# Performance work log

Hardware: AMD Instinct MI355X
Metric: run time of the kernel (lower is better)

The kernel has to match this reference:

```python
import jax, jax.numpy as jnp
import numpy as np

B, P, CIN = 512, 64, 512       # batch, h*w feature positions, resnet18 channels
HID, EMB, NCLS, T = 512, 512, 96, 30


def setup_inputs() -> dict:
    key = jax.random.key(0)
    ks = jax.random.split(key, 16)
    s = 0.02
    return {
        "features": jax.random.normal(ks[0], (B, P, CIN), jnp.float32),
        "targets": jax.random.randint(ks[1], (B, T), 0, NCLS),
        "max_length": T,
        "Wfc": jax.random.normal(ks[2], (HID, CIN), jnp.float32) * s,
        "bfc": jnp.zeros((HID,), jnp.float32),
        "emb_table": jax.random.normal(ks[3], (NCLS, EMB), jnp.float32) * s,
        "Wa": jax.random.normal(ks[4], (HID, HID + EMB), jnp.float32) * s,
        "ba": jnp.zeros((HID,), jnp.float32),
        "Wc": jax.random.normal(ks[5], (HID, HID + EMB), jnp.float32) * s,
        "bc": jnp.zeros((HID,), jnp.float32),
        "Wih": jax.random.normal(ks[6], (4 * HID, HID), jnp.float32) * s,
        "Whh": jax.random.normal(ks[7], (4 * HID, HID), jnp.float32) * s,
        "bih": jnp.zeros((4 * HID,), jnp.float32),
        "bhh": jnp.zeros((4 * HID,), jnp.float32),
        "Wo": jax.random.normal(ks[8], (NCLS, HID), jnp.float32) * s,
        "bo": jnp.zeros((NCLS,), jnp.float32),
    }


def reference(features, targets, max_length, Wfc, bfc, emb_table, Wa, ba,
              Wc, bc, Wih, Whh, bih, bhh, Wo, bo):
    b = features.shape[0]
    hid = Wfc.shape[0]
    feats = features @ Wfc.T + bfc                       # [b, P, hid]
    # teacher forcing: input at t=0 is token 0, then targets[:, t-1]
    in_ids = jnp.concatenate(
        [jnp.zeros((b, 1), targets.dtype), targets[:, : max_length - 1]], axis=1)
    emb_seq = emb_table[in_ids].transpose(1, 0, 2)       # [T, b, emb]

    def step(carry, emb):
        h, c = carry
        # first softmax is over the hidden dim (as in the original module)
        a = jax.nn.softmax(jnp.concatenate([h, emb], -1) @ Wa.T + ba, axis=-1)  # [b,hid]
        scores = jnp.einsum('bph,bh->bp', feats, a)      # [b, P]
        w = jax.nn.softmax(scores, axis=-1)
        ctx = jnp.einsum('bp,bph->bh', w, feats)         # [b, hid]
        x = jnp.concatenate([emb, ctx], -1) @ Wc.T + bc  # [b, hid]
        gates = x @ Wih.T + bih + h @ Whh.T + bhh        # [b, 4*hid]
        i, f, g, o = jnp.split(gates, 4, axis=-1)        # torch gate order i,f,g,o
        c_new = jax.nn.sigmoid(f) * c + jax.nn.sigmoid(i) * jnp.tanh(g)
        h_new = jax.nn.sigmoid(o) * jnp.tanh(c_new)
        out = h_new @ Wo.T + bo                          # [b, ncls]
        return (h_new, c_new), out

    h0 = jnp.zeros((b, hid), feats.dtype)
    (_, _), outs = jax.lax.scan(step, (h0, h0), emb_seq)
    return outs.transpose(1, 0, 2)                       # [b, T, ncls]
```

## Files before the change

kernel.cpp:

```cpp
#include <hip/hip_runtime.h>
#include <math.h>

static constexpr int BATCH = 512;
static constexpr int PPOS  = 64;
static constexpr int HIDC  = 512;

typedef __attribute__((ext_vector_type(8))) short bf8;
typedef __attribute__((ext_vector_type(4))) short s4v;
typedef __attribute__((ext_vector_type(4))) float f4;

static __device__ __forceinline__ float sigmoidf_(float x) { return 1.f / (1.f + expf(-x)); }

static __device__ __forceinline__ short f2bf(float x) {
  unsigned u = __float_as_uint(x);
  u = u + 0x7FFF + ((u >> 16) & 1);
  return (short)(u >> 16);
}
static __device__ __forceinline__ float bf2f(short s) {
  return __uint_as_float(((unsigned)(unsigned short)s) << 16);
}

__global__ void transpose_k(const float* __restrict__ src, float* __restrict__ dst, int R, int C, int ld) {
  __shared__ float tile[32][33];
  int c0 = blockIdx.x * 32, r0 = blockIdx.y * 32;
  int x = threadIdx.x;
  for (int yy = threadIdx.y; yy < 32; yy += 8) {
    int r = r0 + yy, c = c0 + x;
    if (r < R && c < C) tile[yy][x] = src[(size_t)r * ld + c];
  }
  __syncthreads();
  for (int yy = threadIdx.y; yy < 32; yy += 8) {
    int c = c0 + yy, r = r0 + x;
    if (r < R && c < C) dst[(size_t)c * R + r] = tile[x][yy];
  }
}

__global__ void bfuse_k(const float* __restrict__ Wih, const float* __restrict__ bc,
                        const float* __restrict__ bih, const float* __restrict__ bhh,
                        float* __restrict__ bf) {
  int n = blockIdx.x * 256 + threadIdx.x;
  float s = bih[n] + bhh[n];
  const float* w = Wih + (size_t)n * 512;
  for (int m = 0; m < 512; m++) s += w[m] * bc[m];
  bf[n] = s;
}

__global__ void split_k(const float* __restrict__ src, short* __restrict__ hi, short* __restrict__ lo, int n) {
  int i = blockIdx.x * 256 + threadIdx.x;
  if (i < n) {
    float x = src[i];
    short h = f2bf(x);
    hi[i] = h;
    lo[i] = f2bf(x - bf2f(h));
  }
}

__global__ void fsplit_k(const float* __restrict__ src, short* __restrict__ hi, short* __restrict__ lo) {
  int i = blockIdx.x * 256 + threadIdx.x;
  float4 v = ((const float4*)src)[i];
  float a[4] = {v.x, v.y, v.z, v.w};
  s4v h4, l4;
#pragma unroll
  for (int j = 0; j < 4; j++) {
    short h = f2bf(a[j]);
    h4[j] = h;
    l4[j] = f2bf(a[j] - bf2f(h));
  }
  ((s4v*)hi)[i] = h4;
  ((s4v*)lo)[i] = l4;
}

__global__ void pack_split_k(const float* __restrict__ src, int ld,
                             short* __restrict__ hi, short* __restrict__ lo) {
  int idx = blockIdx.x * 256 + threadIdx.x;
  int j = idx & 7, lane = (idx >> 3) & 63, kf = (idx >> 9) & 15, cg = idx >> 13;
  int n = cg * 16 + (lane & 15);
  int k = kf * 32 + ((lane >> 4) << 3) + j;
  float v = src[(size_t)n * ld + k];
  short h = f2bf(v);
  hi[idx] = h;
  lo[idx] = f2bf(v - bf2f(h));
}

__global__ void build_btg_pack_k(const float* __restrict__ tmp, const float* __restrict__ Whh,
                                 short* __restrict__ hi, short* __restrict__ lo) {
  int idx = blockIdx.x * 256 + threadIdx.x;
  int j = idx & 7, lane = (idx >> 3) & 63, kf = (idx >> 9) & 31, cg = idx >> 14;
  int cp = cg * 16 + (lane & 15);
  int k = kf * 32 + ((lane >> 4) << 3) + j;
  int jj = cp >> 2, g = cp & 3;
  int n = g * 512 + jj;
  float v = (k < 512) ? tmp[(size_t)(512 + k) * 2048 + n] : Whh[(size_t)n * 512 + (k - 512)];
  short h = f2bf(v);
  hi[idx] = h;
  lo[idx] = f2bf(v - bf2f(h));
}

__global__ __launch_bounds__(256) void gemb_k(const float* __restrict__ emb_table, const float* __restrict__ tmp,
                                              const float* __restrict__ bfused, float* __restrict__ Gemb_p) {
  __shared__ float emb_s[4][512];
  int tid = threadIdx.x;
  int n0 = blockIdx.x * 256;
  int e0 = blockIdx.y * 4;
  for (int i = tid; i < 2048; i += 256)
    emb_s[i >> 9][i & 511] = emb_table[(size_t)(e0 + (i >> 9)) * 512 + (i & 511)];
  __syncthreads();
  int n = n0 + tid;
  float acc[4] = {};
  for (int k = 0; k < 512; k++) {
    float w = tmp[(size_t)k * 2048 + n];
#pragma unroll
    for (int e = 0; e < 4; e++) acc[e] += emb_s[e][k] * w;
  }
  int cp = (n & 511) * 4 + (n >> 9);
  float b = bfused[n];
#pragma unroll
  for (int e = 0; e < 4; e++) Gemb_p[(size_t)(e0 + e) * 2048 + cp] = acc[e] + b;
}

__global__ __launch_bounds__(256) void za_k(const float* __restrict__ emb_table, const float* __restrict__ WaT_emb,
                                            const float* __restrict__ ba, float* __restrict__ Za) {
  __shared__ float emb_s[4][512];
  int tid = threadIdx.x;
  int n0 = blockIdx.x * 256;
  int e0 = blockIdx.y * 4;
  for (int i = tid; i < 2048; i += 256)
    emb_s[i >> 9][i & 511] = emb_table[(size_t)(e0 + (i >> 9)) * 512 + (i & 511)];
  __syncthreads();
  int n = n0 + tid;
  float acc[4] = {};
  for (int k = 0; k < 512; k++) {
    float w = WaT_emb[(size_t)k * 512 + n];
#pragma unroll
    for (int e = 0; e < 4; e++) acc[e] += emb_s[e][k] * w;
  }
  float b = ba[n];
#pragma unroll
  for (int e = 0; e < 4; e++) Za[(size_t)(e0 + e) * 512 + n] = acc[e] + b;
}

__global__ __launch_bounds__(256) void feats_mfma_k(const short* __restrict__ Fh, const short* __restrict__ Fl,
                                                    const short* __restrict__ Ph, const short* __restrict__ Pl,
                                                    const float* __restrict__ bias, float* __restrict__ C) {
  int blk = blockIdx.x;
  int xt = (blk >> 3) & 3;
  int ytile = (blk >> 5) * 8 + (blk & 7);
  int row0 = ytile * 64, col0 = xt * 128;
  int tid = threadIdx.x;
  int lane = tid & 63, wave = tid >> 6;
  int wm = (wave & 1) * 32, wn = (wave >> 1) * 64;
  int r15 = lane & 15, q8 = (lane >> 4) * 8;
  const short* a0h = Fh + (size_t)(row0 + wm + r15) * 512 + q8;
  const short* a0l = Fl + (size_t)(row0 + wm + r15) * 512 + q8;
  int cg0 = (col0 + wn) >> 4;
  const short* pbh = Ph + (size_t)cg0 * 8192 + lane * 8;
  const short* pbl = Pl + (size_t)cg0 * 8192 + lane * 8;
  bf8 cah[2], cal[2], cbh[4], cbl[4], nah[2], nal[2], nbh[4], nbl[4];
  cah[0] = *(const bf8*)a0h; cah[1] = *(const bf8*)(a0h + 16 * 512);
  cal[0] = *(const bf8*)a0l; cal[1] = *(const bf8*)(a0l + 16 * 512);
#pragma unroll
  for (int c = 0; c < 4; c++) {
    cbh[c] = *(const bf8*)(pbh + c * 8192);
    cbl[c] = *(const bf8*)(pbl + c * 8192);
  }
  f4 acc[2][4] = {};
#pragma unroll 4
  for (int kt = 0; kt < 16; kt++) {
    if (kt + 1 < 16) {
      int o = (kt + 1) * 32;
      nah[0] = *(const bf8*)(a0h + o); nah[1] = *(const bf8*)(a0h + 16 * 512 + o);
      nal[0] = *(const bf8*)(a0l + o); nal[1] = *(const bf8*)(a0l + 16 * 512 + o);
#pragma unroll
      for (int c = 0; c < 4; c++) {
        nbh[c] = *(const bf8*)(pbh + c * 8192 + (kt + 1) * 512);
        nbl[c] = *(const bf8*)(pbl + c * 8192 + (kt + 1) * 512);
      }
    }
#pragma unroll
    for (int r = 0; r < 2; r++)
#pragma unroll
      for (int c = 0; c < 4; c++) {
        acc[r][c] = __builtin_amdgcn_mfma_f32_16x16x32_bf16(cah[r], cbh[c], acc[r][c], 0, 0, 0);
        acc[r][c] = __builtin_amdgcn_mfma_f32_16x16x32_bf16(cal[r], cbh[c], acc[r][c], 0, 0, 0);
        acc[r][c] = __builtin_amdgcn_mfma_f32_16x16x32_bf16(cah[r], cbl[c], acc[r][c], 0, 0, 0);
      }
#pragma unroll
    for (int r = 0; r < 2; r++) { cah[r] = nah[r]; cal[r] = nal[r]; }
#pragma unroll
    for (int c = 0; c < 4; c++) { cbh[c] = nbh[c]; cbl[c] = nbl[c]; }
  }
#pragma unroll
  for (int r = 0; r < 2; r++)
#pragma unroll
    for (int c = 0; c < 4; c++) {
      int col = col0 + wn + c * 16 + r15;
      float bv = bias[col];
#pragma unroll
      for (int i = 0; i < 4; i++) {
        int row = row0 + wm + r * 16 + (lane >> 4) * 4 + i;
        C[(size_t)row * 512 + col] = acc[r][c][i] + bv;
      }
    }
}

__global__ __launch_bounds__(256) void tmp_mfma_k(const float* __restrict__ A,
                                                  const short* __restrict__ BTh, const short* __restrict__ BTl,
                                                  float* __restrict__ C) {
  __shared__ short Ah[2][64][40], Al[2][64][40], Bh[2][128][40], Bl[2][128][40];
  int row0 = blockIdx.y * 64, col0 = blockIdx.x * 128;
  int tid = threadIdx.x;
  int lane = tid & 63, wave = tid >> 6;
  int wm = (wave & 1) * 32, wn = (wave >> 1) * 64;
  int r15 = lane & 15, q8 = (lane >> 4) * 8;
  int smA = tid >> 2, skA = (tid & 3) * 8;
  int smB = tid >> 1, skB = (tid & 1) * 16;
  const float* Ap = A + (size_t)(row0 + smA) * 512 + skA;
  const short* Bhp = BTh + (size_t)(col0 + smB) * 512 + skB;
  const short* Blp = BTl + (size_t)(col0 + smB) * 512 + skB;
  float4 a0 = *(const float4*)Ap, a1 = *(const float4*)(Ap + 4);
  bf8 bh0 = *(const bf8*)Bhp, bh1 = *(const bf8*)(Bhp + 8);
  bf8 bl0 = *(const bf8*)Blp, bl1 = *(const bf8*)(Blp + 8);
  f4 acc[2][4] = {};
  for (int kt = 0; kt < 16; kt++) {
    int buf = kt & 1;
    {
      float av[8] = {a0.x, a0.y, a0.z, a0.w, a1.x, a1.y, a1.z, a1.w};
      bf8 ahv, alv;
#pragma unroll
      for (int i = 0; i < 8; i++) {
        short h = f2bf(av[i]);
        ahv[i] = h;
        alv[i] = f2bf(av[i] - bf2f(h));
      }
      *(bf8*)&Ah[buf][smA][skA] = ahv;
      *(bf8*)&Al[buf][smA][skA] = alv;
      *(bf8*)&Bh[buf][smB][skB] = bh0;
      *(bf8*)&Bh[buf][smB][skB + 8] = bh1;
      *(bf8*)&Bl[buf][smB][skB] = bl0;
      *(bf8*)&Bl[buf][smB][skB + 8] = bl1;
    }
    if (kt + 1 < 16) {
      Ap += 32; Bhp += 32; Blp += 32;
      a0 = *(const float4*)Ap; a1 = *(const float4*)(Ap + 4);
      bh0 = *(const bf8*)Bhp; bh1 = *(const bf8*)(Bhp + 8);
      bl0 = *(const bf8*)Blp; bl1 = *(const bf8*)(Blp + 8);
    }
    __syncthreads();
    bf8 fah[2], fal[2], fbh[4], fbl[4];
#pragma unroll
    for (int r = 0; r < 2; r++) {
      fah[r] = *(const bf8*)&Ah[buf][wm + r * 16 + r15][q8];
      fal[r] = *(const bf8*)&Al[buf][wm + r * 16 + r15][q8];
    }
#pragma unroll
    for (int c = 0; c < 4; c++) {
      fbh[c] = *(const bf8*)&Bh[buf][wn + c * 16 + r15][q8];
      fbl[c] = *(const bf8*)&Bl[buf][wn + c * 16 + r15][q8];
    }
#pragma unroll
    for (int r = 0; r < 2; r++)
#pragma unroll
      for (int c = 0; c < 4; c++) {
        acc[r][c] = __builtin_amdgcn_mfma_f32_16x16x32_bf16(fah[r], fbh[c], acc[r][c], 0, 0, 0);
        acc[r][c] = __builtin_amdgcn_mfma_f32_16x16x32_bf16(fal[r], fbh[c], acc[r][c], 0, 0, 0);
        acc[r][c] = __builtin_amdgcn_mfma_f32_16x16x32_bf16(fah[r], fbl[c], acc[r][c], 0, 0, 0);
      }
  }
#pragma unroll
  for (int r = 0; r < 2; r++)
#pragma unroll
    for (int c = 0; c < 4; c++) {
      int col = col0 + wn + c * 16 + r15;
#pragma unroll
      for (int i = 0; i < 4; i++) {
        int row = row0 + wm + r * 16 + (lane >> 4) * 4 + i;
        C[(size_t)row * 2048 + col] = acc[r][c][i];
      }
    }
}

__global__ __launch_bounds__(256) void z_mfma_k(const short* __restrict__ h_hi, const short* __restrict__ h_lo,
                                                const short* __restrict__ Ph, const short* __restrict__ Pl,
                                                float* __restrict__ zbuf) {
  int tid = threadIdx.x;
  int lane = tid & 63, wave = tid >> 6;
  int wm = (wave & 1) * 16, wn = (wave >> 1) * 16;
  int r15 = lane & 15, q4 = (lane >> 4) * 4, q8 = (lane >> 4) * 8;
  int row0 = blockIdx.y * 32, col0 = blockIdx.x * 32;
  int kz = blockIdx.z * 256;
  const short* ah = h_hi + (size_t)(row0 + wm + r15) * 512 + kz + q8;
  const short* al = h_lo + (size_t)(row0 + wm + r15) * 512 + kz + q8;
  int cg = (col0 + wn) >> 4;
  const short* pbh = Ph + (size_t)cg * 8192 + (size_t)blockIdx.z * 4096 + lane * 8;
  const short* pbl = Pl + (size_t)cg * 8192 + (size_t)blockIdx.z * 4096 + lane * 8;
  bf8 cah = *(const bf8*)ah, cal = *(const bf8*)al;
  bf8 cbh = *(const bf8*)pbh, cbl = *(const bf8*)pbl;
  bf8 nah, nal, nbh, nbl;
  f4 acc = {};
#pragma unroll
  for (int kt = 0; kt < 8; kt++) {
    if (kt + 1 < 8) {
      nah = *(const bf8*)(ah + (kt + 1) * 32);
      nal = *(const bf8*)(al + (kt + 1) * 32);
      nbh = *(const bf8*)(pbh + (kt + 1) * 512);
      nbl = *(const bf8*)(pbl + (kt + 1) * 512);
    }
    acc = __builtin_amdgcn_mfma_f32_16x16x32_bf16(cah, cbh, acc, 0, 0, 0);
    acc = __builtin_amdgcn_mfma_f32_16x16x32_bf16(cal, cbh, acc, 0, 0, 0);
    acc = __builtin_amdgcn_mfma_f32_16x16x32_bf16(cah, cbl, acc, 0, 0, 0);
    cah = nah; cal = nal; cbh = nbh; cbl = nbl;
  }
  float* zo = zbuf + (size_t)blockIdx.z * (512 * 512);
  int col = col0 + wn + r15;
#pragma unroll
  for (int i = 0; i < 4; i++)
    zo[(size_t)(row0 + wm + q4 + i) * 512 + col] = acc[i];
}

__global__ __launch_bounds__(512) void attn_fin_k(const float* __restrict__ zbuf,
                                                  const int* __restrict__ targets, int t, int T,
                                                  const float* __restrict__ Za, const float* __restrict__ feats,
                                                  short* __restrict__ ctx_hi, short* __restrict__ ctx_lo) {
  __shared__ float a_s[512];
  __shared__ float redm[8], reds[8];
  __shared__ float sc_s[64];
  __shared__ float w_s[64];
  __shared__ float cpart[8][512];
  int tid = threadIdx.x;
  int wid = tid >> 6, lane = tid & 63;
  int b = blockIdx.x;
  int id = (t == 0) ? 0 : targets[b * T + t - 1];

  const float4* fbase = (const float4*)(feats + (size_t)b * PPOS * 512);
  float4 f1[8], f2[8];
#pragma unroll
  for (int q = 0; q < 8; q++) {
    int p = wid * 8 + q;
    f1[q] = fbase[(size_t)p * 128 + lane];
    f2[q] = fbase[(size_t)p * 128 + 64 + lane];
  }

  float zv = zbuf[(size_t)b * 512 + tid] + zbuf[(size_t)(512 * 512) + b * 512 + tid]
           + Za[(size_t)id * 512 + tid];
  float m = zv;
#pragma unroll
  for (int off = 32; off; off >>= 1) m = fmaxf(m, __shfl_xor(m, off, 64));
  if (lane == 0) redm[wid] = m;
  __syncthreads();
  float M = redm[0];
#pragma unroll
  for (int w = 1; w < 8; w++) M = fmaxf(M, redm[w]);
  float e = expf(zv - M);
  float s = e;
#pragma unroll
  for (int off = 32; off; off >>= 1) s += __shfl_xor(s, off, 64);
  if (lane == 0) reds[wid] = s;
  __syncthreads();
  float S = 0.f;
#pragma unroll
  for (int w = 0; w < 8; w++) S += reds[w];
  a_s[tid] = e * (1.f / S);
  __syncthreads();

  float4 a1 = ((const float4*)a_s)[lane];
  float4 a2 = ((const float4*)a_s)[lane + 64];
#pragma unroll
  for (int q = 0; q < 8; q++) {
    float d = f1[q].x * a1.x + f1[q].y * a1.y + f1[q].z * a1.z + f1[q].w * a1.w
            + f2[q].x * a2.x + f2[q].y * a2.y + f2[q].z * a2.z + f2[q].w * a2.w;
#pragma unroll
    for (int off = 32; off; off >>= 1) d += __shfl_xor(d, off, 64);
    if (lane == 0) sc_s[wid * 8 + q] = d;
  }
  __syncthreads();

  if (wid == 0) {
    float v = sc_s[lane];
    float mm = v;
#pragma unroll
    for (int off = 32; off; off >>= 1) mm = fmaxf(mm, __shfl_xor(mm, off, 64));
    float ee = expf(v - mm);
    float ss = ee;
#pragma unroll
    for (int off = 32; off; off >>= 1) ss += __shfl_xor(ss, off, 64);
    w_s[lane] = ee / ss;
  }
  __syncthreads();

  float4 c1 = {0.f, 0.f, 0.f, 0.f}, c2 = {0.f, 0.f, 0.f, 0.f};
#pragma unroll
  for (int q = 0; q < 8; q++) {
    float wp = w_s[wid * 8 + q];
    c1.x += wp * f1[q].x; c1.y += wp * f1[q].y; c1.z += wp * f1[q].z; c1.w += wp * f1[q].w;
    c2.x += wp * f2[q].x; c2.y += wp * f2[q].y; c2.z += wp * f2[q].z; c2.w += wp * f2[q].w;
  }
  ((float4*)&cpart[wid][0])[lane] = c1;
  ((float4*)&cpart[wid][256])[lane] = c2;
  __syncthreads();

  float acc = 0.f;
#pragma unroll
  for (int w = 0; w < 8; w++) acc += cpart[w][tid];
  short hh = f2bf(acc);
  ctx_hi[(size_t)b * 512 + tid] = hh;
  ctx_lo[(size_t)b * 512 + tid] = f2bf(acc - bf2f(hh));
}

__global__ __launch_bounds__(256) void gates_mfma_k(const short* __restrict__ ctx_hi, const short* __restrict__ ctx_lo,
                                                    const short* __restrict__ h_hi_in, const short* __restrict__ h_lo_in,
                                                    const int* __restrict__ targets, int t, int T,
                                                    const short* __restrict__ Ph, const short* __restrict__ Pl,
                                                    const float* __restrict__ Gemb_p,
                                                    float* __restrict__ cbuf, float* __restrict__ h_new,
                                                    short* __restrict__ h_hi_out, short* __restrict__ h_lo_out) {
  __shared__ short Ah[2][32][72], Al[2][32][72];
  __shared__ float Cs[32][68];
  int tid = threadIdx.x;
  int lane = tid & 63, wave = tid >> 6;
  int wn = wave * 16;
  int r15 = lane & 15, q8 = (lane >> 4) * 8;
  int row0 = blockIdx.y * 32, col0 = blockIdx.x * 64;
  int smA = tid >> 3, skA = (tid & 7) * 8;
  const short* actx_h = ctx_hi + (size_t)(row0 + smA) * 512;
  const short* actx_l = ctx_lo + (size_t)(row0 + smA) * 512;
  const short* ahst_h = h_hi_in + (size_t)(row0 + smA) * 512;
  const short* ahst_l = h_lo_in + (size_t)(row0 + smA) * 512;
  int cg = (col0 >> 4) + wave;
  const short* pbh = Ph + (size_t)cg * 16384 + lane * 8;
  const short* pbl = Pl + (size_t)cg * 16384 + lane * 8;
  bf8 ah = *(const bf8*)(actx_h + skA), al = *(const bf8*)(actx_l + skA);
  bf8 bhc[2], blc[2], bhn[2], bln[2];
#pragma unroll
  for (int ks = 0; ks < 2; ks++) {
    bhc[ks] = *(const bf8*)(pbh + ks * 512);
    blc[ks] = *(const bf8*)(pbl + ks * 512);
  }
  f4 acc[2] = {};
#pragma unroll 2
  for (int kt = 0; kt < 16; kt++) {
    int buf = kt & 1;
    *(bf8*)&Ah[buf][smA][skA] = ah;
    *(bf8*)&Al[buf][smA][skA] = al;
    if (kt + 1 < 16) {
      int kk = (kt + 1) * 64 + skA;
      if (kk < 512) {
        ah = *(const bf8*)(actx_h + kk);
        al = *(const bf8*)(actx_l + kk);
      } else {
        ah = *(const bf8*)(ahst_h + kk - 512);
        al = *(const bf8*)(ahst_l + kk - 512);
      }
#pragma unroll
      for (int ks = 0; ks < 2; ks++) {
        bhn[ks] = *(const bf8*)(pbh + ((kt + 1) * 2 + ks) * 512);
        bln[ks] = *(const bf8*)(pbl + ((kt + 1) * 2 + ks) * 512);
      }
    }
    __syncthreads();
#pragma unroll
    for (int ks = 0; ks < 2; ks++) {
      bf8 fah[2], fal[2];
#pragma unroll
      for (int r = 0; r < 2; r++) {
        fah[r] = *(const bf8*)&Ah[buf][r * 16 + r15][ks * 32 + q8];
        fal[r] = *(const bf8*)&Al[buf][r * 16 + r15][ks * 32 + q8];
      }
#pragma unroll
      for (int r = 0; r < 2; r++) {
        acc[r] = __builtin_amdgcn_mfma_f32_16x16x32_bf16(fah[r], bhc[ks], acc[r], 0, 0, 0);
        acc[r] = __builtin_amdgcn_mfma_f32_16x16x32_bf16(fal[r], bhc[ks], acc[r], 0, 0, 0);
        acc[r] = __builtin_amdgcn_mfma_f32_16x16x32_bf16(fah[r], blc[ks], acc[r], 0, 0, 0);
      }
    }
#pragma unroll
    for (int ks = 0; ks < 2; ks++) { bhc[ks] = bhn[ks]; blc[ks] = bln[ks]; }
  }
#pragma unroll
  for (int r = 0; r < 2; r++)
#pragma unroll
    for (int i = 0; i < 4; i++)
      Cs[r * 16 + (lane >> 4) * 4 + i][wn + r15] = acc[r][i];
  __syncthreads();
#pragma unroll
  for (int it = 0; it < 2; it++) {
    int idx = it * 256 + tid;
    int row = idx >> 4, jj = idx & 15;
    int b = row0 + row;
    int jg = (col0 >> 2) + jj;
    int id = (t == 0) ? 0 : targets[b * T + t - 1];
    float4 g4 = *(const float4*)(Gemb_p + (size_t)id * 2048 + col0 + jj * 4);
    float ig = sigmoidf_(Cs[row][jj * 4 + 0] + g4.x);
    float fg = sigmoidf_(Cs[row][jj * 4 + 1] + g4.y);
    float gg = tanhf(Cs[row][jj * 4 + 2] + g4.z);
    float og = sigmoidf_(Cs[row][jj * 4 + 3] + g4.w);
    float cn = fg * cbuf[(size_t)b * 512 + jg] + ig * gg;
    float hn = og * tanhf(cn);
    cbuf[(size_t)b * 512 + jg] = cn;
    h_new[(size_t)b * 512 + jg] = hn;
    short hh = f2bf(hn);
    h_hi_out[(size_t)b * 512 + jg] = hh;
    h_lo_out[(size_t)b * 512 + jg] = f2bf(hn - bf2f(hh));
  }
}

__global__ __launch_bounds__(256) void out_gemm_k(const float* __restrict__ h_hist, const float* __restrict__ WoT,
                                                  const float* __restrict__ bo, float* __restrict__ out, int T) {
  __shared__ float As[16][68];
  __shared__ float Bs[16][96];
  int tid = threadIdx.x;
  int tx = tid & 15, ty = tid >> 4;
  int row0 = blockIdx.x * 64;
  float acc[4][6] = {};
  for (int k0 = 0; k0 < 512; k0 += 16) {
    {
      int r = tid >> 2;
      int kk = (tid & 3) * 4;
      float4 v = *(const float4*)(h_hist + (size_t)(row0 + r) * 512 + k0 + kk);
      As[kk + 0][r] = v.x; As[kk + 1][r] = v.y; As[kk + 2][r] = v.z; As[kk + 3][r] = v.w;
    }
#pragma unroll
    for (int i = 0; i < 6; i++) {
      int e = tid + 256 * i;
      int kb = e / 96, n = e - kb * 96;
      Bs[kb][n] = WoT[(size_t)(k0 + kb) * 96 + n];
    }
    __syncthreads();
#pragma unroll
    for (int q = 0; q < 16; q++) {
      float av[4], bvv[6];
#pragma unroll
      for (int i = 0; i < 4; i++) av[i] = As[q][ty * 4 + i];
#pragma unroll
      for (int j = 0; j < 6; j++) bvv[j] = Bs[q][tx * 6 + j];
#pragma unroll
      for (int i = 0; i < 4; i++)
#pragma unroll
        for (int j = 0; j < 6; j++) acc[i][j] += av[i] * bvv[j];
    }
    __syncthreads();
  }
#pragma unroll
  for (int i = 0; i < 4; i++)
#pragma unroll
    for (int j = 0; j < 6; j++) {
      int row = row0 + ty * 4 + i;
      int tt = row >> 9, bb = row & 511;
      int cc = tx * 6 + j;
      out[((size_t)bb * T + tt) * 96 + cc] = acc[i][j] + bo[cc];
    }
}

extern "C" void kernel_launch(void* const* d_in, const int* in_sizes, int n_in,
                              void* d_out, int out_size, void* d_ws, size_t ws_size,
                              hipStream_t stream) {
  const float* features  = (const float*)d_in[0];
  const int*   targets   = (const int*)d_in[1];
  const float* Wfc       = (const float*)d_in[3];
  const float* bfc       = (const float*)d_in[4];
  const float* emb_table = (const float*)d_in[5];
  const float* Wa        = (const float*)d_in[6];
  const float* ba        = (const float*)d_in[7];
  const float* Wc        = (const float*)d_in[8];
  const float* bc        = (const float*)d_in[9];
  const float* Wih       = (const float*)d_in[10];
  const float* Whh       = (const float*)d_in[11];
  const float* bih       = (const float*)d_in[12];
  const float* bhh       = (const float*)d_in[13];
  const float* Wo        = (const float*)d_in[14];
  const float* bo        = (const float*)d_in[15];
  float* out = (float*)d_out;
  int T = in_sizes[1] / BATCH;

  char* base = (char*)d_ws;
  auto alloc = [&](size_t bytes) -> char* {
    char* p = base;
    base += (bytes + 255) & ~(size_t)255;
    return p;
  };
  float* feats   = (float*)alloc((size_t)BATCH * PPOS * HIDC * 4);
  short* f_hi    = (short*)alloc((size_t)BATCH * PPOS * HIDC * 2);
  short* f_lo    = (short*)alloc((size_t)BATCH * PPOS * HIDC * 2);
  float* WaT_emb = (float*)alloc(512 * 512 * 4);
  float* WcT     = (float*)alloc(1024 * 512 * 4);
  float* tmp     = (float*)alloc((size_t)1024 * 2048 * 4);
  short* Wih_hi  = (short*)alloc((size_t)2048 * 512 * 2);
  short* Wih_lo  = (short*)alloc((size_t)2048 * 512 * 2);
  short* PBTg_hi = (short*)alloc((size_t)2048 * 1024 * 2);
  short* PBTg_lo = (short*)alloc((size_t)2048 * 1024 * 2);
  short* Pfc_hi  = (short*)alloc(512 * 512 * 2);
  short* Pfc_lo  = (short*)alloc(512 * 512 * 2);
  short* Pwa_hi  = (short*)alloc(512 * 512 * 2);
  short* Pwa_lo  = (short*)alloc(512 * 512 * 2);
  float* Gemb_p  = (float*)alloc(96 * 2048 * 4);
  float* Za      = (float*)alloc(96 * 512 * 4);
  float* bfused  = (float*)alloc(2048 * 4);
  float* WoT     = (float*)alloc(512 * 96 * 4);
  float* cbuf    = (float*)alloc(BATCH * HIDC * 4);
  float* zbuf    = (float*)alloc((size_t)2 * BATCH * HIDC * 4);
  short* ctx_hi  = (short*)alloc(BATCH * HIDC * 2);
  short* ctx_lo  = (short*)alloc(BATCH * HIDC * 2);
  short* h_hi    = (short*)alloc(BATCH * HIDC * 2);
  short* h_lo    = (short*)alloc(BATCH * HIDC * 2);
  float* h_hist  = (float*)alloc((size_t)T * BATCH * HIDC * 4);

  dim3 tb(32, 8);
  transpose_k<<<dim3(16, 16), tb, 0, stream>>>(Wa + 512, WaT_emb, 512, 512, 1024);
  transpose_k<<<dim3(32, 16), tb, 0, stream>>>(Wc, WcT, 512, 1024, 1024);
  transpose_k<<<dim3(16, 3),  tb, 0, stream>>>(Wo, WoT, 96, 512, 512);

  split_k<<<(2048 * 512) / 256, 256, 0, stream>>>(Wih, Wih_hi, Wih_lo, 2048 * 512);
  pack_split_k<<<(512 * 512) / 256, 256, 0, stream>>>(Wfc, 512, Pfc_hi, Pfc_lo);
  pack_split_k<<<(512 * 512) / 256, 256, 0, stream>>>(Wa, 1024, Pwa_hi, Pwa_lo);
  fsplit_k<<<(BATCH * PPOS * HIDC / 4) / 256, 256, 0, stream>>>(features, f_hi, f_lo);

  tmp_mfma_k<<<dim3(16, 16), 256, 0, stream>>>(WcT, Wih_hi, Wih_lo, tmp);

  bfuse_k<<<8, 256, 0, stream>>>(Wih, bc, bih, bhh, bfused);
  build_btg_pack_k<<<(2048 * 1024) / 256, 256, 0, stream>>>(tmp, Whh, PBTg_hi, PBTg_lo);
  gemb_k<<<dim3(8, 24), 256, 0, stream>>>(emb_table, tmp, bfused, Gemb_p);
  za_k<<<dim3(2, 24), 256, 0, stream>>>(emb_table, WaT_emb, ba, Za);

  feats_mfma_k<<<2048, 256, 0, stream>>>(f_hi, f_lo, Pfc_hi, Pfc_lo, bfc, feats);

  hipMemsetAsync(cbuf, 0, (size_t)BATCH * HIDC * 4, stream);
  hipMemsetAsync(h_hi, 0, (size_t)BATCH * HIDC * 2, stream);
  hipMemsetAsync(h_lo, 0, (size_t)BATCH * HIDC * 2, stream);

  for (int t = 0; t < T; t++) {
    float* h_new = h_hist + (size_t)t * BATCH * HIDC;
    z_mfma_k<<<dim3(16, 16, 2), 256, 0, stream>>>(h_hi, h_lo, Pwa_hi, Pwa_lo, zbuf);
    attn_fin_k<<<512, 512, 0, stream>>>(zbuf, targets, t, T, Za, feats, ctx_hi, ctx_lo);
    gates_mfma_k<<<dim3(32, 16), 256, 0, stream>>>(ctx_hi, ctx_lo, h_hi, h_lo, targets, t, T,
                                                   PBTg_hi, PBTg_lo, Gemb_p, cbuf, h_new, h_hi, h_lo);
  }
  out_gemm_k<<<(T * BATCH) / 64, 256, 0, stream>>>(h_hist, WoT, bo, out, T);
}
```

Baseline: 1.448 ms.

## Stage MFMA A-operands via direct global-to-LDS loads with XOR swizzle

Three MFMA kernels (feats, z, gates) now load the A operand (hi/lo bf16 split) straight from global memory into double-buffered shared memory with global_load_lds. Each kernel then reads its fragments from an XOR-swizzled layout, which replaces per-lane register loads or register-staged LDS stores. The aim is to cut VGPR pressure and load-issue overhead and to avoid LDS bank conflicts, since padding is dropped in favour of the swizzle. In exchange, feats and z gain a __syncthreads per k-iteration, and correctness depends on the async LDS load being complete at the barrier.

New measurement: 1.469 ms. About the same (+1.4%).

```diff
diff --git a/kernel.cpp b/kernel.cpp
--- a/kernel.cpp
+++ b/kernel.cpp
@@ -18,6 +18,11 @@
 }
 static __device__ __forceinline__ float bf2f(short s) {
   return __uint_as_float(((unsigned)(unsigned short)s) << 16);
+}
+
+static __device__ __forceinline__ void gld16(const short* g, short* l) {
+  __builtin_amdgcn_global_load_lds((const __attribute__((address_space(1))) unsigned int*)g,
+                                   (__attribute__((address_space(3))) unsigned int*)l, 16, 0, 0);
 }
 
 __global__ void transpose_k(const float* __restrict__ src, float* __restrict__ dst, int R, int C, int ld) {
@@ -142,6 +147,7 @@
 __global__ __launch_bounds__(256) void feats_mfma_k(const short* __restrict__ Fh, const short* __restrict__ Fl,
                                                     const short* __restrict__ Ph, const short* __restrict__ Pl,
                                                     const float* __restrict__ bias, float* __restrict__ C) {
+  __shared__ short Ah[2][64][32], Al[2][64][32];
   int blk = blockIdx.x;
   int xt = (blk >> 3) & 3;
   int ytile = (blk >> 5) * 8 + (blk & 7);
@@ -149,43 +155,52 @@
   int tid = threadIdx.x;
   int lane = tid & 63, wave = tid >> 6;
   int wm = (wave & 1) * 32, wn = (wave >> 1) * 64;
-  int r15 = lane & 15, q8 = (lane >> 4) * 8;
-  const short* a0h = Fh + (size_t)(row0 + wm + r15) * 512 + q8;
-  const short* a0l = Fl + (size_t)(row0 + wm + r15) * 512 + q8;
+  int r15 = lane & 15;
+  int srow = 16 * wave + (lane >> 2);
+  int sg = (lane & 3) ^ (srow & 3);
+  const short* gAh = Fh + (size_t)(row0 + srow) * 512 + (sg << 3);
+  const short* gAl = Fl + (size_t)(row0 + srow) * 512 + (sg << 3);
   int cg0 = (col0 + wn) >> 4;
   const short* pbh = Ph + (size_t)cg0 * 8192 + lane * 8;
   const short* pbl = Pl + (size_t)cg0 * 8192 + lane * 8;
-  bf8 cah[2], cal[2], cbh[4], cbl[4], nah[2], nal[2], nbh[4], nbl[4];
-  cah[0] = *(const bf8*)a0h; cah[1] = *(const bf8*)(a0h + 16 * 512);
-  cal[0] = *(const bf8*)a0l; cal[1] = *(const bf8*)(a0l + 16 * 512);
+  bf8 cbh[4], cbl[4], nbh[4], nbl[4];
 #pragma unroll
   for (int c = 0; c < 4; c++) {
     cbh[c] = *(const bf8*)(pbh + c * 8192);
     cbl[c] = *(const bf8*)(pbl + c * 8192);
   }
+  gld16(gAh, &Ah[0][16 * wave][0]);
+  gld16(gAl, &Al[0][16 * wave][0]);
+  __syncthreads();
   f4 acc[2][4] = {};
-#pragma unroll 4
   for (int kt = 0; kt < 16; kt++) {
+    int buf = kt & 1;
     if (kt + 1 < 16) {
-      int o = (kt + 1) * 32;
-      nah[0] = *(const bf8*)(a0h + o); nah[1] = *(const bf8*)(a0h + 16 * 512 + o);
-      nal[0] = *(const bf8*)(a0l + o); nal[1] = *(const bf8*)(a0l + 16 * 512 + o);
+      gld16(gAh + (kt + 1) * 32, &Ah[buf ^ 1][16 * wave][0]);
+      gld16(gAl + (kt + 1) * 32, &Al[buf ^ 1][16 * wave][0]);
 #pragma unroll
       for (int c = 0; c < 4; c++) {
         nbh[c] = *(const bf8*)(pbh + c * 8192 + (kt + 1) * 512);
         nbl[c] = *(const bf8*)(pbl + c * 8192 + (kt + 1) * 512);
       }
     }
+    bf8 fah[2], fal[2];
+#pragma unroll
+    for (int r = 0; r < 2; r++) {
+      int row = wm + r * 16 + r15;
+      int off = row * 64 + ((((lane >> 4) ^ (r15 & 3)) << 4));
+      fah[r] = *(const bf8*)((const char*)&Ah[buf][0][0] + off);
+      fal[r] = *(const bf8*)((const char*)&Al[buf][0][0] + off);
+    }
 #pragma unroll
     for (int r = 0; r < 2; r++)
 #pragma unroll
       for (int c = 0; c < 4; c++) {
-        acc[r][c] = __builtin_amdgcn_mfma_f32_16x16x32_bf16(cah[r], cbh[c], acc[r][c], 0, 0, 0);
-        acc[r][c] = __builtin_amdgcn_mfma_f32_16x16x32_bf16(cal[r], cbh[c], acc[r][c], 0, 0, 0);
-        acc[r][c] = __builtin_amdgcn_mfma_f32_16x16x32_bf16(cah[r], cbl[c], acc[r][c], 0, 0, 0);
-      }
-#pragma unroll
-    for (int r = 0; r < 2; r++) { cah[r] = nah[r]; cal[r] = nal[r]; }
+        acc[r][c] = __builtin_amdgcn_mfma_f32_16x16x32_bf16(fah[r], cbh[c], acc[r][c], 0, 0, 0);
+        acc[r][c] = __builtin_amdgcn_mfma_f32_16x16x32_bf16(fal[r], cbh[c], acc[r][c], 0, 0, 0);
+        acc[r][c] = __builtin_amdgcn_mfma_f32_16x16x32_bf16(fah[r], cbl[c], acc[r][c], 0, 0, 0);
+      }
+    __syncthreads();
 #pragma unroll
     for (int c = 0; c < 4; c++) { cbh[c] = nbh[c]; cbl[c] = nbl[c]; }
   }
@@ -282,33 +297,54 @@
 __global__ __launch_bounds__(256) void z_mfma_k(const short* __restrict__ h_hi, const short* __restrict__ h_lo,
                                                 const short* __restrict__ Ph, const short* __restrict__ Pl,
                                                 float* __restrict__ zbuf) {
+  __shared__ short Ah[2][32][64], Al[2][32][64];
   int tid = threadIdx.x;
   int lane = tid & 63, wave = tid >> 6;
   int wm = (wave & 1) * 16, wn = (wave >> 1) * 16;
-  int r15 = lane & 15, q4 = (lane >> 4) * 4, q8 = (lane >> 4) * 8;
+  int r15 = lane & 15, q4 = (lane >> 4) * 4;
   int row0 = blockIdx.y * 32, col0 = blockIdx.x * 32;
   int kz = blockIdx.z * 256;
-  const short* ah = h_hi + (size_t)(row0 + wm + r15) * 512 + kz + q8;
-  const short* al = h_lo + (size_t)(row0 + wm + r15) * 512 + kz + q8;
+  int srow = 8 * wave + (lane >> 3);
+  int sg = (lane & 7) ^ (srow & 7);
+  const short* gAh = h_hi + (size_t)(row0 + srow) * 512 + kz + (sg << 3);
+  const short* gAl = h_lo + (size_t)(row0 + srow) * 512 + kz + (sg << 3);
   int cg = (col0 + wn) >> 4;
   const short* pbh = Ph + (size_t)cg * 8192 + (size_t)blockIdx.z * 4096 + lane * 8;
   const short* pbl = Pl + (size_t)cg * 8192 + (size_t)blockIdx.z * 4096 + lane * 8;
-  bf8 cah = *(const bf8*)ah, cal = *(const bf8*)al;
-  bf8 cbh = *(const bf8*)pbh, cbl = *(const bf8*)pbl;
-  bf8 nah, nal, nbh, nbl;
+  bf8 bhc[2], blc[2], bhn[2], bln[2];
+#pragma unroll
+  for (int ks = 0; ks < 2; ks++) {
+    bhc[ks] = *(const bf8*)(pbh + ks * 512);
+    blc[ks] = *(const bf8*)(pbl + ks * 512);
+  }
+  gld16(gAh, &Ah[0][8 * wave][0]);
+  gld16(gAl, &Al[0][8 * wave][0]);
+  __syncthreads();
   f4 acc = {};
-#pragma unroll
-  for (int kt = 0; kt < 8; kt++) {
-    if (kt + 1 < 8) {
-      nah = *(const bf8*)(ah + (kt + 1) * 32);
-      nal = *(const bf8*)(al + (kt + 1) * 32);
-      nbh = *(const bf8*)(pbh + (kt + 1) * 512);
-      nbl = *(const bf8*)(pbl + (kt + 1) * 512);
-    }
-    acc = __builtin_amdgcn_mfma_f32_16x16x32_bf16(cah, cbh, acc, 0, 0, 0);
-    acc = __builtin_amdgcn_mfma_f32_16x16x32_bf16(cal, cbh, acc, 0, 0, 0);
-    acc = __builtin_amdgcn_mfma_f32_16x16x32_bf16(cah, cbl, acc, 0, 0, 0);
-    cah = nah; cal = nal; cbh = nbh; cbl = nbl;
+  for (int kt = 0; kt < 4; kt++) {
+    int buf = kt & 1;
+    if (kt + 1 < 4) {
+      gld16(gAh + (kt + 1) * 64, &Ah[buf ^ 1][8 * wave][0]);
+      gld16(gAl + (kt + 1) * 64, &Al[buf ^ 1][8 * wave][0]);
+#pragma unroll
+      for (int ks = 0; ks < 2; ks++) {
+        bhn[ks] = *(const bf8*)(pbh + ((kt + 1) * 2 + ks) * 512);
+        bln[ks] = *(const bf8*)(pbl + ((kt + 1) * 2 + ks) * 512);
+      }
+    }
+#pragma unroll
+    for (int ks = 0; ks < 2; ks++) {
+      int row = wm + r15;
+      int off = row * 128 + (((ks * 4 + (lane >> 4)) ^ (r15 & 7)) << 4);
+      bf8 fah = *(const bf8*)((const char*)&Ah[buf][0][0] + off);
+      bf8 fal = *(const bf8*)((const char*)&Al[buf][0][0] + off);
+      acc = __builtin_amdgcn_mfma_f32_16x16x32_bf16(fah, bhc[ks], acc, 0, 0, 0);
+      acc = __builtin_amdgcn_mfma_f32_16x16x32_bf16(fal, bhc[ks], acc, 0, 0, 0);
+      acc = __builtin_amdgcn_mfma_f32_16x16x32_bf16(fah, blc[ks], acc, 0, 0, 0);
+    }
+    __syncthreads();
+#pragma unroll
+    for (int ks = 0; ks < 2; ks++) { bhc[ks] = bhn[ks]; blc[ks] = bln[ks]; }
   }
   float* zo = zbuf + (size_t)blockIdx.z * (512 * 512);
   int col = col0 + wn + r15;
@@ -413,57 +449,56 @@
                                                     const float* __restrict__ Gemb_p,
                                                     float* __restrict__ cbuf, float* __restrict__ h_new,
                                                     short* __restrict__ h_hi_out, short* __restrict__ h_lo_out) {
-  __shared__ short Ah[2][32][72], Al[2][32][72];
+  __shared__ short Ah[2][32][64], Al[2][32][64];
   __shared__ float Cs[32][68];
   int tid = threadIdx.x;
   int lane = tid & 63, wave = tid >> 6;
   int wn = wave * 16;
-  int r15 = lane & 15, q8 = (lane >> 4) * 8;
+  int r15 = lane & 15;
   int row0 = blockIdx.y * 32, col0 = blockIdx.x * 64;
-  int smA = tid >> 3, skA = (tid & 7) * 8;
-  const short* actx_h = ctx_hi + (size_t)(row0 + smA) * 512;
-  const short* actx_l = ctx_lo + (size_t)(row0 + smA) * 512;
-  const short* ahst_h = h_hi_in + (size_t)(row0 + smA) * 512;
-  const short* ahst_l = h_lo_in + (size_t)(row0 + smA) * 512;
+  int srow = 8 * wave + (lane >> 3);
+  int sg = (lane & 7) ^ (srow & 7);
+  const short* gCh = ctx_hi + (size_t)(row0 + srow) * 512 + (sg << 3);
+  const short* gCl = ctx_lo + (size_t)(row0 + srow) * 512 + (sg << 3);
+  const short* gHh = h_hi_in + (size_t)(row0 + srow) * 512 + (sg << 3);
+  const short* gHl = h_lo_in + (size_t)(row0 + srow) * 512 + (sg << 3);
   int cg = (col0 >> 4) + wave;
   const short* pbh = Ph + (size_t)cg * 16384 + lane * 8;
   const short* pbl = Pl + (size_t)cg * 16384 + lane * 8;
-  bf8 ah = *(const bf8*)(actx_h + skA), al = *(const bf8*)(actx_l + skA);
   bf8 bhc[2], blc[2], bhn[2], bln[2];
 #pragma unroll
   for (int ks = 0; ks < 2; ks++) {
     bhc[ks] = *(const bf8*)(pbh + ks * 512);
     blc[ks] = *(const bf8*)(pbl + ks * 512);
   }
+  gld16(gCh, &Ah[0][8 * wave][0]);
+  gld16(gCl, &Al[0][8 * wave][0]);
+  __syncthreads();
   f4 acc[2] = {};
-#pragma unroll 2
   for (int kt = 0; kt < 16; kt++) {
     int buf = kt & 1;
-    *(bf8*)&Ah[buf][smA][skA] = ah;
-    *(bf8*)&Al[buf][smA][skA] = al;
     if (kt + 1 < 16) {
-      int kk = (kt + 1) * 64 + skA;
-      if (kk < 512) {
-        ah = *(const bf8*)(actx_h + kk);
-        al = *(const bf8*)(actx_l + kk);
-      } else {
-        ah = *(const bf8*)(ahst_h + kk - 512);
-        al = *(const bf8*)(ahst_l + kk - 512);
-      }
+      int kt1 = kt + 1;
+      const short* sh = (kt1 < 8) ? gCh : gHh;
+      const short* sl = (kt1 < 8) ? gCl : gHl;
+      int ko = (kt1 < 8) ? kt1 * 64 : (kt1 - 8) * 64;
+      gld16(sh + ko, &Ah[buf ^ 1][8 * wave][0]);
+      gld16(sl + ko, &Al[buf ^ 1][8 * wave][0]);
 #pragma unroll
       for (int ks = 0; ks < 2; ks++) {
-        bhn[ks] = *(const bf8*)(pbh + ((kt + 1) * 2 + ks) * 512);
-        bln[ks] = *(const bf8*)(pbl + ((kt + 1) * 2 + ks) * 512);
-      }
-    }
-    __syncthreads();
+        bhn[ks] = *(const bf8*)(pbh + (kt1 * 2 + ks) * 512);
+        bln[ks] = *(const bf8*)(pbl + (kt1 * 2 + ks) * 512);
+      }
+    }
 #pragma unroll
     for (int ks = 0; ks < 2; ks++) {
       bf8 fah[2], fal[2];
 #pragma unroll
       for (int r = 0; r < 2; r++) {
-        fah[r] = *(const bf8*)&Ah[buf][r * 16 + r15][ks * 32 + q8];
-        fal[r] = *(const bf8*)&Al[buf][r * 16 + r15][ks * 32 + q8];
+        int row = r * 16 + r15;
+        int off = row * 128 + (((ks * 4 + (lane >> 4)) ^ (r15 & 7)) << 4);
+        fah[r] = *(const bf8*)((const char*)&Ah[buf][0][0] + off);
+        fal[r] = *(const bf8*)((const char*)&Al[buf][0][0] + off);
       }
 #pragma unroll
       for (int r = 0; r < 2; r++) {
@@ -472,6 +507,7 @@
         acc[r] = __builtin_amdgcn_mfma_f32_16x16x32_bf16(fah[r], blc[ks], acc[r], 0, 0, 0);
       }
     }
+    __syncthreads();
 #pragma unroll
     for (int ks = 0; ks < 2; ks++) { bhc[ks] = bhn[ks]; blc[ks] = bln[ks]; }
   }
```
